# Kernel tuning notes

Hardware: AMD Instinct MI355X
Metric: run time of the kernel (lower is better)

Reference implementation:

```python
import jax, jax.numpy as jnp
import numpy as np

# Static hyperparameters (match init_kwargs)
PAD = 4          # one_side_pad_length
KL = 9           # kernel_size (= 2*PAD + 1 so L_out == output_size with stride 1)
STRIDE = 1
NLC = 8          # num_sparse_LC
OUT = 4096       # output_size


def _repeat_lengths():
    padded = OUT + 2 * PAD                      # 4104
    rough = padded // NLC                       # 513
    lens = []
    total = 0
    for i in range(NLC):
        if i == NLC - 1:
            cover = OUT - total
        else:
            cover = rough - 2 * PAD
        lens.append(cover)
        total += cover
    return lens                                  # [505]*7 + [561]


def setup_inputs() -> dict:
    key = jax.random.key(0)
    k1, k2, k3 = jax.random.split(key, 3)
    x = jax.random.normal(k1, (8, 2, 4, 64, 4096), dtype=jnp.float32)
    # weight: (dim_d, dim_k, out, in, num_sparse_LC, 1, kernel_size)
    weight = jax.random.normal(k2, (2, 4, 64, 64, 8, 1, 9), dtype=jnp.float32) * 0.05
    # conv_bias_param: (dim_d, dim_k, out, num_sparse_LC, 1)
    conv_bias_param = jax.random.normal(k3, (2, 4, 64, 8, 1), dtype=jnp.float32) * 0.02
    return {"x": x, "weight": weight, "conv_bias_param": conv_bias_param}


def reference(x, weight, conv_bias_param):
    # x: (b, d, k, in, L)
    x_pad = jnp.pad(x, ((0, 0), (0, 0), (0, 0), (0, 0), (PAD, PAD)))
    # unfold(-1, KL, 1): x_unf[..., l, f] = x_pad[..., l + f]; shape (b,d,k,in,OUT,KL)
    x_unf = jnp.stack([x_pad[..., f:f + OUT] for f in range(KL)], axis=-1)
    lens = _repeat_lengths()
    outs = []
    start = 0
    for i in range(NLC):  # small fixed loop over segments (avoids repeated-weight materialization)
        ln = lens[i]
        w = weight[:, :, :, :, i, 0, :]                 # (d, k, o, in, kl)
        xs = x_unf[:, :, :, :, start:start + ln, :]     # (b, d, k, in, ln, kl)
        o = jnp.einsum('dkoif,bdkilf->bdkol', w, xs)    # (b, d, k, o, ln)
        o = o + conv_bias_param[None, :, :, :, i, :]    # bias broadcasts over b and l
        outs.append(o)
        start += ln
    return jnp.concatenate(outs, axis=-1)               # (b, d, k, o, OUT)
```

## Files before the change

### kernel.cpp

```cpp
#include <hip/hip_runtime.h>

typedef __attribute__((ext_vector_type(8))) short bf16x8;
typedef __attribute__((ext_vector_type(4))) float f32x4;

#define WT2_BYTES (8ull * 8 * 9 * 8192)

#define AS1C(p) ((const __attribute__((address_space(1))) void*)(p))
#define AS3(p)  ((__attribute__((address_space(3))) void*)(p))

static __device__ __forceinline__ ushort f2bf(float f) {
    union { float f; unsigned u; } v; v.f = f;
    unsigned r = v.u + 0x7FFF + ((v.u >> 16) & 1);
    return (ushort)(r >> 16);
}
static __device__ __forceinline__ unsigned cvtpk(float a, float b) {
    unsigned r;
    asm("v_cvt_pk_bf16_f32 %0, %1, %2" : "=v"(r) : "v"(a), "v"(b));
    return r;
}

__global__ __launch_bounds__(256) void wprep3_kernel(const float* __restrict__ w,
                                                     ushort* __restrict__ wt) {
    __shared__ float raw[4608];
    __shared__ ushort row[72 * 64];
    int bid = blockIdx.x;
    int dk = bid >> 6, o = bid & 63;
    const float* src = w + (size_t)bid * 4608;
    int t = threadIdx.x;
    #pragma unroll
    for (int j = 0; j < 18; ++j) raw[t + 256 * j] = src[t + 256 * j];
    __syncthreads();
    int osw = o & 7;
    #pragma unroll
    for (int p = 0; p < 18; ++p) {
        int idx = t + 256 * p;
        int cf = idx >> 6, i = idx & 63;
        int c = cf / 9, f = cf - c * 9;
        row[cf * 64 + ((i >> 3) ^ osw) * 8 + (i & 7)] = f2bf(raw[i * 72 + c * 9 + f]);
    }
    __syncthreads();
    char* wb = (char*)wt + (size_t)dk * 8 * 9 * 8192 + o * 128;
    #pragma unroll
    for (int q = 0; q < 3; ++q) {
        int idx = q * 256 + t;
        if (idx < 576) {
            int cf = idx >> 3, cc = idx & 7;
            *(uint4*)(wb + (size_t)cf * 8192 + cc * 16) = *(const uint4*)&row[cf * 64 + cc * 8];
        }
    }
}

__global__ __launch_bounds__(512, 4) void conv11_kernel(
    const float* __restrict__ x, const ushort* __restrict__ wt,
    const float* __restrict__ bias, float* __restrict__ out)
{
    __shared__ __align__(16) ushort XL[264 * 64];
    __shared__ __align__(16) ushort WL[4 * 4096];

    int bid = blockIdx.x;
    int b = bid / 136, rem = bid - b * 136;
    int dk = rem / 17, tile = rem - dk * 17;
    int c, lt;
    if (tile < 14) { c = tile >> 1; lt = tile & 1; } else { c = 7; lt = tile - 14; }
    int Sc = 505 * c, lb = lt << 8;
    int V = ((c == 7) ? 561 : 505) - lb; if (V > 256) V = 256;
    int bdk = b * 8 + dk;
    int R0 = Sc + lb;

    int t = threadIdx.x, lane = t & 63, wv = t >> 6;
    int ln16 = lane & 15, g = lane >> 4;
    int wr = wv >> 1, wc = wv & 1;
    int Lw = wr << 6, Ow = wc << 5;

    int lq = t & 63, ig = t >> 6;
    const float* xb = x + (size_t)bdk * 64 * 4096;
    float4 v[8];
    bool edge = (R0 < 4) || (R0 > 3836);
    if (!edge) {
        const float* xp = xb + (size_t)ig * 8 * 4096 + (R0 - 4 + lq * 4);
        #pragma unroll
        for (int j = 0; j < 8; ++j)
            v[j] = *(const float4*)(xp + (size_t)j * 4096);
    } else {
        #pragma unroll
        for (int j = 0; j < 8; ++j) {
            float* pv = (float*)&v[j];
            #pragma unroll
            for (int k = 0; k < 4; ++k) {
                int xr = R0 - 4 + lq * 4 + k;
                bool ok = (xr >= 0) && (xr < 4096);
                int xc = ok ? xr : 0;
                pv[k] = ok ? xb[(size_t)(ig * 8 + j) * 4096 + xc] : 0.0f;
            }
        }
    }
    float hv[8]; int rh = 0, igh = 0;
    if (t < 64) {
        rh = 256 + (t >> 3);
        igh = t & 7;
        int xr = R0 - 4 + rh;
        bool okh = xr < 4096;
        int xc = okh ? xr : 0;
        const float* xh = xb + (size_t)igh * 8 * 4096 + xc;
        #pragma unroll
        for (int j = 0; j < 8; ++j) hv[j] = okh ? xh[(size_t)j * 4096] : 0.0f;
    }

    const char* wsl = (const char*)wt + (size_t)(dk * 8 + c) * 9 * 8192;
    auto stageW = [&](int f, int buf) {
        __builtin_amdgcn_global_load_lds(AS1C(wsl + (size_t)f * 8192 + t * 16),
                                         AS3((char*)WL + buf * 8192 + t * 16), 16, 0, 0);
    };
    stageW(0, 0); stageW(1, 1); stageW(2, 2);

    #pragma unroll
    for (int k = 0; k < 4; ++k) {
        int r = lq * 4 + k;
        uint4 A;
        A.x = cvtpk(((const float*)&v[0])[k], ((const float*)&v[1])[k]);
        A.y = cvtpk(((const float*)&v[2])[k], ((const float*)&v[3])[k]);
        A.z = cvtpk(((const float*)&v[4])[k], ((const float*)&v[5])[k]);
        A.w = cvtpk(((const float*)&v[6])[k], ((const float*)&v[7])[k]);
        *(uint4*)((char*)XL + r * 128 + ((ig ^ (r & 7)) * 16)) = A;
    }
    if (t < 64) {
        uint4 A;
        A.x = cvtpk(hv[0], hv[1]); A.y = cvtpk(hv[2], hv[3]);
        A.z = cvtpk(hv[4], hv[5]); A.w = cvtpk(hv[6], hv[7]);
        *(uint4*)((char*)XL + rh * 128 + ((igh ^ (rh & 7)) * 16)) = A;
    }

    f32x4 acc[4][2];
    #pragma unroll
    for (int a0 = 0; a0 < 4; ++a0)
        #pragma unroll
        for (int a1 = 0; a1 < 2; ++a1) acc[a0][a1] = (f32x4){0.f, 0.f, 0.f, 0.f};

    auto tap = [&](int f) {
        int buf = f & 3;
        int rbase = Lw + ln16 + f;
        int swz = rbase & 7;
        #pragma unroll
        for (int s = 0; s < 2; ++s) {
            int cof = ((s * 4 + g) ^ swz) * 16;
            int wof = buf * 8192 + ((s * 4 + g) ^ (ln16 & 7)) * 16;
            bf16x8 av[4], bv[2];
            #pragma unroll
            for (int mf = 0; mf < 4; ++mf)
                av[mf] = *(const bf16x8*)((const char*)XL + (rbase + mf * 16) * 128 + cof);
            #pragma unroll
            for (int nf = 0; nf < 2; ++nf)
                bv[nf] = *(const bf16x8*)((const char*)WL + wof + (Ow + nf * 16 + ln16) * 128);
            #pragma unroll
            for (int mf = 0; mf < 4; ++mf)
                #pragma unroll
                for (int nf = 0; nf < 2; ++nf)
                    acc[mf][nf] = __builtin_amdgcn_mfma_f32_16x16x32_bf16(av[mf], bv[nf], acc[mf][nf], 0, 0, 0);
        }
    };

    asm volatile("s_waitcnt lgkmcnt(0)" ::: "memory");

#define TAPSTEP(N, F, ISSUE) \
    asm volatile("s_waitcnt vmcnt(" #N ")" ::: "memory"); \
    __builtin_amdgcn_s_barrier(); \
    __builtin_amdgcn_sched_barrier(0); \
    if (ISSUE) stageW(F + 3, (F + 3) & 3); \
    tap(F);

    TAPSTEP(2, 0, 1) TAPSTEP(2, 1, 1) TAPSTEP(2, 2, 1) TAPSTEP(2, 3, 1)
    TAPSTEP(2, 4, 1) TAPSTEP(2, 5, 1) TAPSTEP(2, 6, 0) TAPSTEP(1, 7, 0)
    TAPSTEP(0, 8, 0)
#undef TAPSTEP

    float* ob = out + ((size_t)(bdk * 64)) * 4096 + Sc + lb;
    #pragma unroll
    for (int nf = 0; nf < 2; ++nf) {
        int o = Ow + nf * 16 + ln16;
        float bvs = bias[(dk * 64 + o) * 8 + c];
        #pragma unroll
        for (int mf = 0; mf < 4; ++mf) {
            int l = Lw + mf * 16 + g * 4;
            f32x4 vv = acc[mf][nf];
            vv[0] += bvs; vv[1] += bvs; vv[2] += bvs; vv[3] += bvs;
            if (l + 4 <= V) {
                *(f32x4*)(ob + (size_t)o * 4096 + l) = vv;
            } else if (l < V) {
                #pragma unroll
                for (int r = 0; r < 4; ++r)
                    if (l + r < V) ob[(size_t)o * 4096 + l + r] = vv[r];
            }
        }
    }
}

extern "C" void kernel_launch(void* const* d_in, const int* in_sizes, int n_in,
                              void* d_out, int out_size, void* d_ws, size_t ws_size,
                              hipStream_t stream) {
    const float* x    = (const float*)d_in[0];
    const float* wgt  = (const float*)d_in[1];
    const float* bias = (const float*)d_in[2];
    float* out        = (float*)d_out;
    ushort* wt2       = (ushort*)d_ws;

    hipLaunchKernelGGL(wprep3_kernel, dim3(512), dim3(256), 0, stream, wgt, wt2);
    hipLaunchKernelGGL(conv11_kernel, dim3(1088), dim3(512), 0, stream, x, wt2, bias, out);
}
```

Before: 50.54 us.

## Load weight fragments directly into registers instead of staging through LDS

Drops the 4-buffer LDS weight ring filled by global_load_lds, along with its per-tap barriers. Each wave now loads its own B fragments from global memory (L2-resident) into registers, double-buffered across taps. MFMA sections are also bracketed with s_setprio. The goal is to remove the per-tap barriers, cut LDS traffic and free LDS for occupancy. The cost is redundant global loads across waves that share the same weight columns, plus possible stalls on global-load latency, since there is no explicit vmcnt wait before each tap.

```diff
diff --git a/kernel.cpp b/kernel.cpp
--- a/kernel.cpp
+++ b/kernel.cpp
@@ -4,9 +4,6 @@
 typedef __attribute__((ext_vector_type(4))) float f32x4;
 
 #define WT2_BYTES (8ull * 8 * 9 * 8192)
-
-#define AS1C(p) ((const __attribute__((address_space(1))) void*)(p))
-#define AS3(p)  ((__attribute__((address_space(3))) void*)(p))
 
 static __device__ __forceinline__ ushort f2bf(float f) {
     union { float f; unsigned u; } v; v.f = f;
@@ -50,12 +47,11 @@
     }
 }
 
-__global__ __launch_bounds__(512, 4) void conv11_kernel(
+__global__ __launch_bounds__(512, 4) void conv12_kernel(
     const float* __restrict__ x, const ushort* __restrict__ wt,
     const float* __restrict__ bias, float* __restrict__ out)
 {
     __shared__ __align__(16) ushort XL[264 * 64];
-    __shared__ __align__(16) ushort WL[4 * 4096];
 
     int bid = blockIdx.x;
     int b = bid / 136, rem = bid - b * 136;
@@ -107,11 +103,23 @@
     }
 
     const char* wsl = (const char*)wt + (size_t)(dk * 8 + c) * 9 * 8192;
-    auto stageW = [&](int f, int buf) {
-        __builtin_amdgcn_global_load_lds(AS1C(wsl + (size_t)f * 8192 + t * 16),
-                                         AS3((char*)WL + buf * 8192 + t * 16), 16, 0, 0);
+    int wo[2][2];
+    #pragma unroll
+    for (int s = 0; s < 2; ++s)
+        #pragma unroll
+        for (int nf = 0; nf < 2; ++nf)
+            wo[s][nf] = (Ow + nf * 16 + ln16) * 128 + (((s * 4 + g) ^ (ln16 & 7)) * 16);
+
+    bf16x8 w0[2][2], w1[2][2];
+    auto loadW = [&](bf16x8 (&d)[2][2], int f) {
+        const char* bp = wsl + (size_t)f * 8192;
+        #pragma unroll
+        for (int s = 0; s < 2; ++s)
+            #pragma unroll
+            for (int nf = 0; nf < 2; ++nf)
+                d[s][nf] = *(const bf16x8*)(bp + wo[s][nf]);
     };
-    stageW(0, 0); stageW(1, 1); stageW(2, 2);
+    loadW(w0, 0);
 
     #pragma unroll
     for (int k = 0; k < 4; ++k) {
@@ -129,6 +137,10 @@
         A.z = cvtpk(hv[4], hv[5]); A.w = cvtpk(hv[6], hv[7]);
         *(uint4*)((char*)XL + rh * 128 + ((igh ^ (rh & 7)) * 16)) = A;
     }
+    loadW(w1, 1);
+
+    asm volatile("s_waitcnt lgkmcnt(0)" ::: "memory");
+    __syncthreads();
 
     f32x4 acc[4][2];
     #pragma unroll
@@ -136,42 +148,35 @@
         #pragma unroll
         for (int a1 = 0; a1 < 2; ++a1) acc[a0][a1] = (f32x4){0.f, 0.f, 0.f, 0.f};
 
-    auto tap = [&](int f) {
-        int buf = f & 3;
+    auto tap = [&](int f, bf16x8 (&wf)[2][2]) {
         int rbase = Lw + ln16 + f;
         int swz = rbase & 7;
         #pragma unroll
         for (int s = 0; s < 2; ++s) {
             int cof = ((s * 4 + g) ^ swz) * 16;
-            int wof = buf * 8192 + ((s * 4 + g) ^ (ln16 & 7)) * 16;
-            bf16x8 av[4], bv[2];
+            bf16x8 av[4];
             #pragma unroll
             for (int mf = 0; mf < 4; ++mf)
                 av[mf] = *(const bf16x8*)((const char*)XL + (rbase + mf * 16) * 128 + cof);
-            #pragma unroll
-            for (int nf = 0; nf < 2; ++nf)
-                bv[nf] = *(const bf16x8*)((const char*)WL + wof + (Ow + nf * 16 + ln16) * 128);
+            __builtin_amdgcn_s_setprio(1);
             #pragma unroll
             for (int mf = 0; mf < 4; ++mf)
                 #pragma unroll
                 for (int nf = 0; nf < 2; ++nf)
-                    acc[mf][nf] = __builtin_amdgcn_mfma_f32_16x16x32_bf16(av[mf], bv[nf], acc[mf][nf], 0, 0, 0);
+                    acc[mf][nf] = __builtin_amdgcn_mfma_f32_16x16x32_bf16(av[mf], wf[s][nf], acc[mf][nf], 0, 0, 0);
+            __builtin_amdgcn_s_setprio(0);
         }
     };
 
-    asm volatile("s_waitcnt lgkmcnt(0)" ::: "memory");
-
-#define TAPSTEP(N, F, ISSUE) \
-    asm volatile("s_waitcnt vmcnt(" #N ")" ::: "memory"); \
-    __builtin_amdgcn_s_barrier(); \
-    __builtin_amdgcn_sched_barrier(0); \
-    if (ISSUE) stageW(F + 3, (F + 3) & 3); \
-    tap(F);
-
-    TAPSTEP(2, 0, 1) TAPSTEP(2, 1, 1) TAPSTEP(2, 2, 1) TAPSTEP(2, 3, 1)
-    TAPSTEP(2, 4, 1) TAPSTEP(2, 5, 1) TAPSTEP(2, 6, 0) TAPSTEP(1, 7, 0)
-    TAPSTEP(0, 8, 0)
-#undef TAPSTEP
+    tap(0, w0); loadW(w0, 2);
+    tap(1, w1); loadW(w1, 3);
+    tap(2, w0); loadW(w0, 4);
+    tap(3, w1); loadW(w1, 5);
+    tap(4, w0); loadW(w0, 6);
+    tap(5, w1); loadW(w1, 7);
+    tap(6, w0); loadW(w0, 8);
+    tap(7, w1);
+    tap(8, w0);
 
     float* ob = out + ((size_t)(bdk * 64)) * 4096 + Sc + lb;
     #pragma unroll
@@ -204,5 +209,5 @@
     ushort* wt2       = (ushort*)d_ws;
 
     hipLaunchKernelGGL(wprep3_kernel, dim3(512), dim3(256), 0, stream, wgt, wt2);
-    hipLaunchKernelGGL(conv11_kernel, dim3(1088), dim3(512), 0, stream, x, wt2, bias, out);
-}
+    hipLaunchKernelGGL(conv12_kernel, dim3(1088), dim3(512), 0, stream, x, wt2, bias, out);
+}
```

Result: faster. 49.34 us (median of 3 runs) (-2.4%).
